# Performance work log

Hardware: AMD Instinct MI355X
Metric: run time of the kernel (lower is better)

The kernel has to match this reference:

```python
import jax, jax.numpy as jnp
import numpy as np

B, L, S, H, C = 64, 512, 512, 768, 9  # batch, bert subword len, word seq len, hidden, num_classes


def setup_inputs() -> dict:
    key = jax.random.key(0)
    k1, k2, k3 = jax.random.split(key, 3)
    rng = np.random.RandomState(0)
    # per-word subword counts in {1,2,3}; truncate so totals fit in L subword slots
    lens = rng.randint(1, 4, size=(B, S))
    cum = lens.cumsum(axis=1)
    keep = cum <= L
    ids_lens = (lens * keep).astype(np.int32)
    totals = ids_lens.sum(axis=1)
    attention_mask = (np.arange(L)[None, :] < totals[:, None]).astype(np.int32)
    label_mask = ids_lens > 0
    label_ids = (rng.randint(0, C, size=(B, S)) * label_mask).astype(np.int32)
    bert_out = jax.random.normal(k1, (B, L, H), dtype=jnp.float32)
    W = jax.random.normal(k2, (H, C), dtype=jnp.float32) * 0.02
    b = jnp.zeros((C,), dtype=jnp.float32)
    return {
        "bert_out": bert_out,
        "W": W,
        "b": b,
        "attention_mask": jnp.asarray(attention_mask),
        "ids_lens": jnp.asarray(ids_lens),
        "label_ids": jnp.asarray(label_ids),
        "label_mask": jnp.asarray(label_mask),
    }


def reference(bert_out, W, b, attention_mask, ids_lens, label_ids, label_mask):
    Bv, Lv, Hv = bert_out.shape
    Sv = ids_lens.shape[1]
    nseg = Bv * Sv
    am = attention_mask.astype(jnp.int32)
    # subword position within each example's valid region
    sidx = jnp.cumsum(am, axis=1) - 1                       # [B, L]
    # word index for each subword: searchsorted into cumulative word lengths
    ends = jnp.cumsum(ids_lens, axis=1)                     # [B, S]
    widx = jax.vmap(lambda e, s: jnp.searchsorted(e, s, side='right'))(ends, sidx)
    seg = jnp.where(am > 0, widx + jnp.arange(Bv)[:, None] * Sv, nseg)  # pad bucket = nseg
    flat = bert_out.reshape(Bv * Lv, Hv)
    segf = seg.reshape(Bv * Lv)
    sums = jax.ops.segment_sum(flat, segf, num_segments=nseg + 1)[:nseg]
    cnts = jax.ops.segment_sum(jnp.ones((Bv * Lv,), bert_out.dtype), segf,
                               num_segments=nseg + 1)[:nseg]
    mean = sums / jnp.maximum(cnts, 1.0)[:, None]           # segment mean (split().mean(0))
    word_mask = (ids_lens > 0).reshape(nseg)
    embed = jnp.where(word_mask[:, None], mean, 0.0).reshape(Bv, Sv, Hv)  # masked_scatter
    # dropout in eval mode = identity
    logits = embed @ W + b                                  # [B, S, C]
    logp = jax.nn.log_softmax(logits, axis=-1)
    lab = jnp.clip(label_ids, 0, W.shape[1] - 1)
    nll = -jnp.take_along_axis(logp, lab[..., None].astype(jnp.int32), axis=-1)[..., 0]
    valid = label_mask.astype(bert_out.dtype)
    loss = jnp.sum(nll * valid) / jnp.maximum(jnp.sum(valid), 1.0)
    pred = jnp.argmax(logits, axis=-1)
    return loss, pred
```

## Files before the change

### kernel.cpp

```cpp
#include <hip/hip_runtime.h>

#define BB 64
#define LL 512
#define SS 512
#define HH 768
#define CC 9
#define WPB 32
#define NBLK (BB * SS / WPB)
#define MAXROWS (WPB * 3)
#define WTPAD 772
#define RLST 12

template <int CTRL>
__device__ __forceinline__ float dpp_add(float x) {
    int y = __builtin_amdgcn_update_dpp(0, __float_as_int(x), CTRL, 0xf, 0xf, true);
    return x + __int_as_float(y);
}
__device__ __forceinline__ float rsum64(float x) {
    x = dpp_add<0x111>(x);
    x = dpp_add<0x112>(x);
    x = dpp_add<0x114>(x);
    x = dpp_add<0x118>(x);
    x = dpp_add<0x142>(x);
    x = dpp_add<0x143>(x);
    return x;
}

__global__ __launch_bounds__(256) void fused_kernel(
    const float* __restrict__ bert,
    const float* __restrict__ Wm,
    const float* __restrict__ bias,
    const int* __restrict__ ids_lens,
    const int* __restrict__ label_ids,
    float* __restrict__ pred_out,
    float* __restrict__ nll_part,
    float* __restrict__ cnt_part)
{
    __shared__ __align__(16) float WT[CC][WTPAD];
    __shared__ __align__(16) float RLs[MAXROWS][RLST];
    __shared__ int wlen[WPB], woff[WPB];
    __shared__ int s_meta[2];
    __shared__ float red[4];

    int b = blockIdx.x >> 4;
    int q = blockIdx.x & 15;
    int w0 = q * WPB;
    const int* lens = ids_lens + b * SS;

    int t = threadIdx.x, lane = t & 63, wave = t >> 6;

    for (int i = t; i < HH * CC; i += 256) {
        int h = i / CC;
        int c = i - h * CC;
        WT[c][h] = Wm[i];
    }
    if (t < WPB) wlen[t] = lens[w0 + t];

    int part = 0;
    for (int i = t; i < w0; i += 256) part += lens[i];
    float pf = rsum64((float)part);
    if (lane == 63) red[wave] = pf;
    __syncthreads();
    if (t == 0) {
        int start0 = (int)(red[0] + red[1] + red[2] + red[3]);
        int run = 0;
#pragma unroll
        for (int k = 0; k < WPB; k++) { woff[k] = run; run += wlen[k]; }
        s_meta[0] = start0;
        s_meta[1] = run;
    }
    __syncthreads();
    int start0 = s_meta[0];
    int rows_n = s_meta[1];

    int hoff = lane * 4;
    float4 wreg[CC][3];
#pragma unroll
    for (int c = 0; c < CC; c++)
#pragma unroll
        for (int c3 = 0; c3 < 3; c3++)
            wreg[c][c3] = *reinterpret_cast<const float4*>(&WT[c][c3 * 256 + hoff]);

    for (int r = wave; r < rows_n; r += 4) {
        const float* p = bert + ((size_t)(b * LL + start0 + r)) * HH + hoff;
        float4 f0 = *reinterpret_cast<const float4*>(p);
        float4 f1 = *reinterpret_cast<const float4*>(p + 256);
        float4 f2 = *reinterpret_cast<const float4*>(p + 512);

        float acc[CC];
#pragma unroll
        for (int c = 0; c < CC; c++) {
            acc[c] = f0.x * wreg[c][0].x + f0.y * wreg[c][0].y
                   + f0.z * wreg[c][0].z + f0.w * wreg[c][0].w
                   + f1.x * wreg[c][1].x + f1.y * wreg[c][1].y
                   + f1.z * wreg[c][1].z + f1.w * wreg[c][1].w
                   + f2.x * wreg[c][2].x + f2.y * wreg[c][2].y
                   + f2.z * wreg[c][2].z + f2.w * wreg[c][2].w;
        }
#pragma unroll
        for (int c = 0; c < CC; c++) acc[c] = rsum64(acc[c]);

        if (lane == 63) {
            float4 s0; s0.x = acc[0]; s0.y = acc[1]; s0.z = acc[2]; s0.w = acc[3];
            float4 s1; s1.x = acc[4]; s1.y = acc[5]; s1.z = acc[6]; s1.w = acc[7];
            *reinterpret_cast<float4*>(&RLs[r][0]) = s0;
            *reinterpret_cast<float4*>(&RLs[r][4]) = s1;
            RLs[r][8] = acc[8];
        }
    }
    __syncthreads();

    if (t < 64) {
        int k = t;
        bool active = k < WPB;
        int len = active ? wlen[k] : 0;
        int off = active ? woff[k] : 0;

        float s[CC];
#pragma unroll
        for (int c = 0; c < CC; c++) s[c] = 0.0f;
        for (int j = 0; j < len; ++j) {
            const float* p = &RLs[off + j][0];
            float4 a = *reinterpret_cast<const float4*>(p);
            float4 c4 = *reinterpret_cast<const float4*>(p + 4);
            s[0] += a.x;  s[1] += a.y;  s[2] += a.z;  s[3] += a.w;
            s[4] += c4.x; s[5] += c4.y; s[6] += c4.z; s[7] += c4.w;
            s[8] += p[8];
        }
        float inv = 1.0f / (float)(len > 0 ? len : 1);
        float lg[CC];
#pragma unroll
        for (int c = 0; c < CC; c++) lg[c] = s[c] * inv + bias[c];

        float mx = lg[0];
        int arg = 0;
#pragma unroll
        for (int c = 1; c < CC; c++) {
            if (lg[c] > mx) { mx = lg[c]; arg = c; }
        }
        float se = 0.0f;
#pragma unroll
        for (int c = 0; c < CC; c++) se += expf(lg[c] - mx);
        float lse = mx + logf(se);

        int g = b * SS + w0 + (active ? k : 0);
        int lab = label_ids[g];
        lab = lab < 0 ? 0 : (lab > CC - 1 ? CC - 1 : lab);
        float valid = (active && len > 0) ? 1.0f : 0.0f;
        float nll = (lse - lg[lab]) * valid;

        if (active) pred_out[g] = (float)arg;

        float rn = rsum64(nll);
        float rc = rsum64(valid);
        if (t == 63) {
            nll_part[blockIdx.x] = rn;
            cnt_part[blockIdx.x] = rc;
        }
    }
}

__global__ __launch_bounds__(1024) void finalize_kernel(
    const float* __restrict__ nll_part,
    const float* __restrict__ cnt_part,
    float* __restrict__ out_loss) {
    __shared__ float sn[16], sc[16];
    int t = threadIdx.x, lane = t & 63, wave = t >> 6;
    float n = nll_part[t];
    float c = cnt_part[t];
    n = rsum64(n);
    c = rsum64(c);
    if (lane == 63) { sn[wave] = n; sc[wave] = c; }
    __syncthreads();
    if (t == 0) {
        float tn = 0.0f, tc = 0.0f;
#pragma unroll
        for (int i = 0; i < 16; i++) { tn += sn[i]; tc += sc[i]; }
        out_loss[0] = tn / fmaxf(tc, 1.0f);
    }
}

extern "C" void kernel_launch(void* const* d_in, const int* in_sizes, int n_in,
                              void* d_out, int out_size, void* d_ws, size_t ws_size,
                              hipStream_t stream) {
    const float* bert = (const float*)d_in[0];
    const float* Wm   = (const float*)d_in[1];
    const float* bias = (const float*)d_in[2];
    const int* ids_lens  = (const int*)d_in[4];
    const int* label_ids = (const int*)d_in[5];

    float* out = (float*)d_out;

    float* nll_part = (float*)d_ws;
    float* cnt_part = nll_part + NBLK;

    fused_kernel<<<NBLK, 256, 0, stream>>>(bert, Wm, bias, ids_lens, label_ids,
                                           out + 1, nll_part, cnt_part);
    finalize_kernel<<<1, 1024, 0, stream>>>(nll_part, cnt_part, out);
}
```

Measured before the change: 177.6 us.

## Split fused kernel into transpose, row GEMM, and segment pooling kernels

Breaks the fused per-word-chunk kernel into a one-time weight transpose kernel, a uniform row-wise projection kernel over all subword rows, and a pooling kernel that averages the projected logits per word. This removes the per-block weight transpose into shared memory and gives the projection a fixed, regular work layout. In exchange it adds kernel launches, a global round trip for per-row logits, and work on padded rows that were previously skipped.

```diff
diff --git a/kernel.cpp b/kernel.cpp
--- a/kernel.cpp
+++ b/kernel.cpp
@@ -5,11 +5,12 @@
 #define SS 512
 #define HH 768
 #define CC 9
-#define WPB 32
-#define NBLK (BB * SS / WPB)
-#define MAXROWS (WPB * 3)
-#define WTPAD 772
-#define RLST 12
+#define NROWS (BB * LL)
+#define RLS 12
+#define G1 1024
+#define ROWS_PER_BLOCK 32
+#define WPS 64
+#define G2 (BB * SS / WPS)
 
 template <int CTRL>
 __device__ __forceinline__ float dpp_add(float x) {
@@ -26,9 +27,67 @@
     return x;
 }
 
-__global__ __launch_bounds__(256) void fused_kernel(
+__global__ __launch_bounds__(256) void wt_kernel(const float* __restrict__ Wm,
+                                                 float* __restrict__ WT_g) {
+    int e = blockIdx.x * 256 + threadIdx.x;
+    if (e < HH * CC) {
+        int h = e / CC;
+        int c = e - h * CC;
+        WT_g[c * HH + h] = Wm[e];
+    }
+}
+
+__global__ __launch_bounds__(256) void row_gemm_kernel(
     const float* __restrict__ bert,
-    const float* __restrict__ Wm,
+    const float* __restrict__ WT_g,
+    float* __restrict__ RL)
+{
+    int wave = threadIdx.x >> 6;
+    int lane = threadIdx.x & 63;
+    int hoff = lane * 4;
+
+    float4 wreg[CC][3];
+#pragma unroll
+    for (int c = 0; c < CC; c++)
+#pragma unroll
+        for (int c3 = 0; c3 < 3; c3++)
+            wreg[c][c3] = *reinterpret_cast<const float4*>(WT_g + c * HH + c3 * 256 + hoff);
+
+    size_t row0 = (size_t)blockIdx.x * ROWS_PER_BLOCK + wave * 8;
+
+#pragma unroll
+    for (int r = 0; r < 8; ++r) {
+        const float* p = bert + (row0 + r) * HH + hoff;
+        float4 f0 = *reinterpret_cast<const float4*>(p);
+        float4 f1 = *reinterpret_cast<const float4*>(p + 256);
+        float4 f2 = *reinterpret_cast<const float4*>(p + 512);
+
+        float acc[CC];
+#pragma unroll
+        for (int c = 0; c < CC; c++) {
+            acc[c] = f0.x * wreg[c][0].x + f0.y * wreg[c][0].y
+                   + f0.z * wreg[c][0].z + f0.w * wreg[c][0].w
+                   + f1.x * wreg[c][1].x + f1.y * wreg[c][1].y
+                   + f1.z * wreg[c][1].z + f1.w * wreg[c][1].w
+                   + f2.x * wreg[c][2].x + f2.y * wreg[c][2].y
+                   + f2.z * wreg[c][2].z + f2.w * wreg[c][2].w;
+        }
+#pragma unroll
+        for (int c = 0; c < CC; c++) acc[c] = rsum64(acc[c]);
+
+        if (lane == 63) {
+            float* dst = RL + (row0 + r) * RLS;
+            float4 s0; s0.x = acc[0]; s0.y = acc[1]; s0.z = acc[2]; s0.w = acc[3];
+            float4 s1; s1.x = acc[4]; s1.y = acc[5]; s1.z = acc[6]; s1.w = acc[7];
+            *reinterpret_cast<float4*>(dst) = s0;
+            *reinterpret_cast<float4*>(dst + 4) = s1;
+            dst[8] = acc[8];
+        }
+    }
+}
+
+__global__ __launch_bounds__(256) void pool_kernel(
+    const float* __restrict__ RL,
     const float* __restrict__ bias,
     const int* __restrict__ ids_lens,
     const int* __restrict__ label_ids,
@@ -36,25 +95,18 @@
     float* __restrict__ nll_part,
     float* __restrict__ cnt_part)
 {
-    __shared__ __align__(16) float WT[CC][WTPAD];
-    __shared__ __align__(16) float RLs[MAXROWS][RLST];
-    __shared__ int wlen[WPB], woff[WPB];
-    __shared__ int s_meta[2];
+    __shared__ int wlen[WPS], woff[WPS];
     __shared__ float red[4];
-
-    int b = blockIdx.x >> 4;
-    int q = blockIdx.x & 15;
-    int w0 = q * WPB;
+    __shared__ int s_start;
+
+    int b = blockIdx.x >> 3;
+    int s8 = blockIdx.x & 7;
+    int w0 = s8 * WPS;
     const int* lens = ids_lens + b * SS;
 
     int t = threadIdx.x, lane = t & 63, wave = t >> 6;
 
-    for (int i = t; i < HH * CC; i += 256) {
-        int h = i / CC;
-        int c = i - h * CC;
-        WT[c][h] = Wm[i];
-    }
-    if (t < WPB) wlen[t] = lens[w0 + t];
+    if (t < WPS) wlen[t] = lens[w0 + t];
 
     int part = 0;
     for (int i = t; i < w0; i += 256) part += lens[i];
@@ -62,65 +114,24 @@
     if (lane == 63) red[wave] = pf;
     __syncthreads();
     if (t == 0) {
-        int start0 = (int)(red[0] + red[1] + red[2] + red[3]);
         int run = 0;
 #pragma unroll
-        for (int k = 0; k < WPB; k++) { woff[k] = run; run += wlen[k]; }
-        s_meta[0] = start0;
-        s_meta[1] = run;
-    }
-    __syncthreads();
-    int start0 = s_meta[0];
-    int rows_n = s_meta[1];
-
-    int hoff = lane * 4;
-    float4 wreg[CC][3];
-#pragma unroll
-    for (int c = 0; c < CC; c++)
-#pragma unroll
-        for (int c3 = 0; c3 < 3; c3++)
-            wreg[c][c3] = *reinterpret_cast<const float4*>(&WT[c][c3 * 256 + hoff]);
-
-    for (int r = wave; r < rows_n; r += 4) {
-        const float* p = bert + ((size_t)(b * LL + start0 + r)) * HH + hoff;
-        float4 f0 = *reinterpret_cast<const float4*>(p);
-        float4 f1 = *reinterpret_cast<const float4*>(p + 256);
-        float4 f2 = *reinterpret_cast<const float4*>(p + 512);
-
-        float acc[CC];
-#pragma unroll
-        for (int c = 0; c < CC; c++) {
-            acc[c] = f0.x * wreg[c][0].x + f0.y * wreg[c][0].y
-                   + f0.z * wreg[c][0].z + f0.w * wreg[c][0].w
-                   + f1.x * wreg[c][1].x + f1.y * wreg[c][1].y
-                   + f1.z * wreg[c][1].z + f1.w * wreg[c][1].w
-                   + f2.x * wreg[c][2].x + f2.y * wreg[c][2].y
-                   + f2.z * wreg[c][2].z + f2.w * wreg[c][2].w;
-        }
-#pragma unroll
-        for (int c = 0; c < CC; c++) acc[c] = rsum64(acc[c]);
-
-        if (lane == 63) {
-            float4 s0; s0.x = acc[0]; s0.y = acc[1]; s0.z = acc[2]; s0.w = acc[3];
-            float4 s1; s1.x = acc[4]; s1.y = acc[5]; s1.z = acc[6]; s1.w = acc[7];
-            *reinterpret_cast<float4*>(&RLs[r][0]) = s0;
-            *reinterpret_cast<float4*>(&RLs[r][4]) = s1;
-            RLs[r][8] = acc[8];
-        }
+        for (int k = 0; k < WPS; k++) { woff[k] = run; run += wlen[k]; }
+        s_start = (int)(red[0] + red[1] + red[2] + red[3]);
     }
     __syncthreads();
 
     if (t < 64) {
         int k = t;
-        bool active = k < WPB;
-        int len = active ? wlen[k] : 0;
-        int off = active ? woff[k] : 0;
+        int len = wlen[k];
+        int off = s_start + woff[k];
+        const float* base = RL + ((size_t)b * LL + off) * RLS;
 
         float s[CC];
 #pragma unroll
         for (int c = 0; c < CC; c++) s[c] = 0.0f;
         for (int j = 0; j < len; ++j) {
-            const float* p = &RLs[off + j][0];
+            const float* p = base + j * RLS;
             float4 a = *reinterpret_cast<const float4*>(p);
             float4 c4 = *reinterpret_cast<const float4*>(p + 4);
             s[0] += a.x;  s[1] += a.y;  s[2] += a.z;  s[3] += a.w;
@@ -143,13 +154,13 @@
         for (int c = 0; c < CC; c++) se += expf(lg[c] - mx);
         float lse = mx + logf(se);
 
-        int g = b * SS + w0 + (active ? k : 0);
+        int g = b * SS + w0 + k;
         int lab = label_ids[g];
         lab = lab < 0 ? 0 : (lab > CC - 1 ? CC - 1 : lab);
-        float valid = (active && len > 0) ? 1.0f : 0.0f;
+        float valid = (len > 0) ? 1.0f : 0.0f;
         float nll = (lse - lg[lab]) * valid;
 
-        if (active) pred_out[g] = (float)arg;
+        pred_out[g] = (float)arg;
 
         float rn = rsum64(nll);
         float rc = rsum64(valid);
@@ -160,22 +171,20 @@
     }
 }
 
-__global__ __launch_bounds__(1024) void finalize_kernel(
+__global__ __launch_bounds__(512) void finalize_kernel(
     const float* __restrict__ nll_part,
     const float* __restrict__ cnt_part,
     float* __restrict__ out_loss) {
-    __shared__ float sn[16], sc[16];
+    __shared__ float sn[8], sc[8];
     int t = threadIdx.x, lane = t & 63, wave = t >> 6;
-    float n = nll_part[t];
-    float c = cnt_part[t];
-    n = rsum64(n);
-    c = rsum64(c);
+    float n = rsum64(nll_part[t]);
+    float c = rsum64(cnt_part[t]);
     if (lane == 63) { sn[wave] = n; sc[wave] = c; }
     __syncthreads();
     if (t == 0) {
         float tn = 0.0f, tc = 0.0f;
 #pragma unroll
-        for (int i = 0; i < 16; i++) { tn += sn[i]; tc += sc[i]; }
+        for (int i = 0; i < 8; i++) { tn += sn[i]; tc += sc[i]; }
         out_loss[0] = tn / fmaxf(tc, 1.0f);
     }
 }
@@ -191,10 +200,14 @@
 
     float* out = (float*)d_out;
 
-    float* nll_part = (float*)d_ws;
-    float* cnt_part = nll_part + NBLK;
-
-    fused_kernel<<<NBLK, 256, 0, stream>>>(bert, Wm, bias, ids_lens, label_ids,
-                                           out + 1, nll_part, cnt_part);
-    finalize_kernel<<<1, 1024, 0, stream>>>(nll_part, cnt_part, out);
-}
+    float* WT_g     = (float*)d_ws;
+    float* RL       = WT_g + CC * HH;
+    float* nll_part = RL + (size_t)NROWS * RLS;
+    float* cnt_part = nll_part + G2;
+
+    wt_kernel<<<(HH * CC + 255) / 256, 256, 0, stream>>>(Wm, WT_g);
+    row_gemm_kernel<<<G1, 256, 0, stream>>>(bert, WT_g, RL);
+    pool_kernel<<<G2, 256, 0, stream>>>(RL, bias, ids_lens, label_ids,
+                                        out + 1, nll_part, cnt_part);
+    finalize_kernel<<<1, 512, 0, stream>>>(nll_part, cnt_part, out);
+}
```

Result: faster. 168.4 us (-5.1%).
